# Performance work log

Hardware: AMD Instinct MI355X
Metric: run time of the kernel (lower is better)

## Reference

```python
import jax, jax.numpy as jnp
import numpy as np


def gcn_conv(x, row, col, ew, W, b, N):
    # GCNConv: add self-loops (weight 1), symmetric normalization, X @ W, scatter-add, + bias
    loop = jnp.arange(N, dtype=row.dtype)
    r = jnp.concatenate([row, loop])
    c = jnp.concatenate([col, loop])
    w = jnp.concatenate([ew, jnp.ones((N,), dtype=x.dtype)])
    deg = jax.ops.segment_sum(w, c, num_segments=N)
    dinv = jnp.where(deg > 0, jax.lax.rsqrt(deg), 0.0).astype(x.dtype)
    norm = dinv[r] * w * dinv[c]                  # [E+N]
    h = x @ W                                     # [N, out]
    msg = h[r] * norm[:, None]                    # gather + scale
    out = jax.ops.segment_sum(msg, c, num_segments=N)  # scatter-add to targets
    return out + b


def setup_inputs() -> dict:
    key = jax.random.key(0)
    ks = jax.random.split(key, 10)
    N, E, C_in, C_hid, C_out = 65536, 1048576, 16, 64, 2
    x = jax.random.normal(ks[0], (N, C_in), dtype=jnp.float32)
    edge_index = jax.random.randint(ks[1], (2, E), 0, N, dtype=jnp.int64)
    edge_weight = jax.random.uniform(ks[2], (E,), dtype=jnp.float32)
    s = lambda k, sh, fan: jax.random.normal(k, sh, dtype=jnp.float32) / np.sqrt(fan)
    return {
        "x": x,
        "edge_index": edge_index,
        "edge_weight": edge_weight,
        "W1": s(ks[3], (C_in, C_hid), C_in),
        "b1": jnp.zeros((C_hid,), dtype=jnp.float32),
        "W2": s(ks[4], (C_hid, C_hid), C_hid),
        "b2": jnp.zeros((C_hid,), dtype=jnp.float32),
        "Wl": s(ks[5], (C_hid, C_out), C_hid),
        "bl": jnp.zeros((C_out,), dtype=jnp.float32),
    }


def reference(x, edge_index, edge_weight, W1, b1, W2, b2, Wl, bl):
    N = x.shape[0]
    row, col = edge_index[0], edge_index[1]  # source -> target
    h = jax.nn.relu(gcn_conv(x, row, col, edge_weight, W1, b1, N))
    h = jax.nn.relu(gcn_conv(h, row, col, edge_weight, W2, b2, N))
    return h @ Wl + bl
```

## Files before the change

### kernel.cpp

```cpp
#include <hip/hip_runtime.h>
#include <hip/hip_fp16.h>

#define CHUNK 4096
#define SEGCAP 6144

__device__ __forceinline__ unsigned pack_h2(float a, float b) {
    __half2 h = __floats2half2_rn(a, b);
    return *reinterpret_cast<unsigned*>(&h);
}

__device__ __forceinline__ void scan_boff(const int* __restrict__ bsum, int nb,
                                          int* boff) {
    int t = threadIdx.x;
    int v = (t < nb) ? bsum[t] : 0;
    boff[t] = v;
    __syncthreads();
    for (int o = 1; o < 256; o <<= 1) {
        int x = (t >= o) ? boff[t - o] : 0;
        __syncthreads();
        boff[t] += x;
        __syncthreads();
    }
    int excl = boff[t] - v;
    __syncthreads();
    boff[t] = excl;
    __syncthreads();
}

__global__ __launch_bounds__(256) void s1_hist(const int* __restrict__ col,
                                               int* __restrict__ F, int E, int nsb) {
    __shared__ int cnt[256];
    int t = threadIdx.x, b = blockIdx.x;
    cnt[t] = 0;
    __syncthreads();
    int s = b * CHUNK, e = min(E, s + CHUNK);
    for (int i = s + t; i < e; i += 256) atomicAdd(&cnt[col[i] >> 8], 1);
    __syncthreads();
    F[t * nsb + b] = cnt[t];
}

__global__ void scanF1(int* __restrict__ F, int* __restrict__ bsum, int n) {
    __shared__ int sd[256];
    int t = threadIdx.x, i = blockIdx.x * 256 + t;
    int v = (i < n) ? F[i] : 0;
    sd[t] = v;
    __syncthreads();
    for (int o = 1; o < 256; o <<= 1) {
        int x = (t >= o) ? sd[t - o] : 0;
        __syncthreads();
        sd[t] += x;
        __syncthreads();
    }
    if (i < n) F[i] = sd[t] - v;
    if (t == 255) bsum[blockIdx.x] = sd[255];
}

__global__ __launch_bounds__(256) void s3_scatter(const int* __restrict__ col,
                                                  const int* __restrict__ row,
                                                  const float* __restrict__ ew,
                                                  const int* __restrict__ F,
                                                  const int* __restrict__ bsum,
                                                  int2* __restrict__ tmp, int E, int nsb) {
    __shared__ int boff[256];
    __shared__ int off[256];
    __shared__ int cnt[256];
    __shared__ int lofs[256];
    __shared__ int cur[256];
    __shared__ int2 ed[CHUNK];
    __shared__ unsigned short perm[CHUNK];
    int t = threadIdx.x, b = blockIdx.x;
    scan_boff(bsum, nsb, boff);
    off[t] = F[t * nsb + b] + boff[t];
    cnt[t] = 0; cur[t] = 0;
    __syncthreads();
    int s = b * CHUNK;
    int m = min(E - s, CHUNK);
    for (int i = t; i < m; i += 256) {
        int c = col[s + i];
        ed[i] = make_int2((row[s + i] & 0xFFFF) | (c << 16), __float_as_int(ew[s + i]));
        atomicAdd(&cnt[c >> 8], 1);
    }
    __syncthreads();
    int v = cnt[t];
    lofs[t] = v;
    __syncthreads();
    for (int o = 1; o < 256; o <<= 1) {
        int x = (t >= o) ? lofs[t - o] : 0;
        __syncthreads();
        lofs[t] += x;
        __syncthreads();
    }
    int excl = lofs[t] - v;
    __syncthreads();
    lofs[t] = excl;
    __syncthreads();
    for (int i = t; i < m; i += 256) {
        int bk = ((unsigned)ed[i].x) >> 24;
        int rk = atomicAdd(&cur[bk], 1);
        perm[lofs[bk] + rk] = (unsigned short)i;
    }
    __syncthreads();
    for (int p = t; p < m; p += 256) {
        int2 v2 = ed[perm[p]];
        int bk = ((unsigned)v2.x) >> 24;
        tmp[off[bk] + (p - lofs[bk])] = v2;
    }
}

__global__ __launch_bounds__(256) void s4_fine(const int2* __restrict__ tmp,
                                               const int* __restrict__ F,
                                               const int* __restrict__ bsum,
                                               unsigned* __restrict__ pack,
                                               float* __restrict__ dinv,
                                               int* __restrict__ start,
                                               const float* __restrict__ x,
                                               const float* __restrict__ W1,
                                               __half* __restrict__ g1,
                                               int n, int E, int nsb, int nbuck) {
    __shared__ int   boff[256];
    __shared__ int   fcnt[256];
    __shared__ float fdeg[256];
    __shared__ int   foff[256];
    __shared__ int   fcur[256];
    __shared__ float Ws[16 * 64];
    __shared__ int2  seg[SEGCAP];
    __shared__ unsigned short perm[SEGCAP];
    int t = threadIdx.x, b = blockIdx.x;
    scan_boff(bsum, nsb, boff);
    reinterpret_cast<float4*>(Ws)[t] = reinterpret_cast<const float4*>(W1)[t];
    fcnt[t] = 0; fdeg[t] = 0.f; fcur[t] = 0;
    __syncthreads();
    int segS = F[b * nsb] + boff[b];
    int segE = (b == nbuck - 1) ? E : (F[(b + 1) * nsb] + boff[b + 1]);
    int m = segE - segS;
    if (m <= SEGCAP) {
        for (int i = t; i < m; i += 256) seg[i] = tmp[segS + i];
        __syncthreads();
        for (int i = t; i < m; i += 256) {
            int2 v = seg[i];
            int f = (v.x >> 16) & 255;
            atomicAdd(&fcnt[f], 1);
            atomicAdd(&fdeg[f], __int_as_float(v.y));
        }
        __syncthreads();
        int val = fcnt[t];
        foff[t] = val;
        __syncthreads();
        for (int o = 1; o < 256; o <<= 1) {
            int xk = (t >= o) ? foff[t - o] : 0;
            __syncthreads();
            foff[t] += xk;
            __syncthreads();
        }
        int excl = foff[t] - val;
        __syncthreads();
        foff[t] = excl;
        __syncthreads();
        for (int i = t; i < m; i += 256) {
            int f = (seg[i].x >> 16) & 255;
            int rk = atomicAdd(&fcur[f], 1);
            perm[foff[f] + rk] = (unsigned short)i;
        }
        __syncthreads();
        for (int p = t; p < m; p += 256) {
            int2 v = seg[perm[p]];
            __half hw = __float2half_rn(__int_as_float(v.y));
            pack[segS + p] = (unsigned)(v.x & 0xFFFF) |
                             ((unsigned)*reinterpret_cast<unsigned short*>(&hw) << 16);
        }
    } else {
        for (int i = segS + t; i < segE; i += 256) {
            int2 v = tmp[i];
            int f = (v.x >> 16) & 255;
            atomicAdd(&fcnt[f], 1);
            atomicAdd(&fdeg[f], __int_as_float(v.y));
        }
        __syncthreads();
        int val = fcnt[t];
        foff[t] = val;
        __syncthreads();
        for (int o = 1; o < 256; o <<= 1) {
            int xk = (t >= o) ? foff[t - o] : 0;
            __syncthreads();
            foff[t] += xk;
            __syncthreads();
        }
        int excl = foff[t] - val;
        __syncthreads();
        foff[t] = excl;
        __syncthreads();
        for (int i = segS + t; i < segE; i += 256) {
            int2 v = tmp[i];
            int f = (v.x >> 16) & 255;
            int rk = atomicAdd(&fcur[f], 1);
            __half hw = __float2half_rn(__int_as_float(v.y));
            pack[segS + foff[f] + rk] = (unsigned)(v.x & 0xFFFF) |
                             ((unsigned)*reinterpret_cast<unsigned short*>(&hw) << 16);
        }
    }
    int c = (b << 8) | t;
    float di = rsqrtf(fdeg[t] + 1.0f);
    if (c < n) {
        dinv[c]  = di;
        start[c] = segS + foff[t];
    }
    if (b == nbuck - 1 && t == 255) start[n] = E;
    if (c >= n) return;
    float xv[16];
    const float4* xr = reinterpret_cast<const float4*>(x + (size_t)c * 16);
#pragma unroll
    for (int i = 0; i < 4; ++i)
        *reinterpret_cast<float4*>(&xv[i * 4]) = xr[i];
    uint2* orow = reinterpret_cast<uint2*>(g1 + ((size_t)c << 6));
    for (int jb = 0; jb < 16; ++jb) {
        float4 acc = make_float4(0.f, 0.f, 0.f, 0.f);
#pragma unroll
        for (int k = 0; k < 16; ++k) {
            float hk = xv[k];
            const float4 wv = *reinterpret_cast<const float4*>(&Ws[k * 64 + jb * 4]);
            acc.x += hk * wv.x; acc.y += hk * wv.y;
            acc.z += hk * wv.z; acc.w += hk * wv.w;
        }
        uint2 st;
        st.x = pack_h2(acc.x * di, acc.y * di);
        st.y = pack_h2(acc.z * di, acc.w * di);
        orow[jb] = st;
    }
}

__global__ __launch_bounds__(256) void gemm_hid(const float* __restrict__ h,
                                                const float* __restrict__ W,
                                                const float* __restrict__ dinv,
                                                __half* __restrict__ out, int n) {
    __shared__ float Ws[64 * 64];
    int t = threadIdx.x;
#pragma unroll
    for (int i = 0; i < 16; ++i) Ws[i * 256 + t] = W[i * 256 + t];
    __syncthreads();
    int node = blockIdx.x * 256 + t;
    if (node >= n) return;
    float hv[64];
    const float4* hr = reinterpret_cast<const float4*>(h + ((size_t)node << 6));
#pragma unroll
    for (int i = 0; i < 16; ++i)
        *reinterpret_cast<float4*>(&hv[i * 4]) = hr[i];
    float di = dinv[node];
    uint2* orow = reinterpret_cast<uint2*>(out + ((size_t)node << 6));
    for (int jb = 0; jb < 16; ++jb) {
        float4 acc = make_float4(0.f, 0.f, 0.f, 0.f);
#pragma unroll
        for (int k = 0; k < 64; ++k) {
            float hk = hv[k];
            const float4 wv = *reinterpret_cast<const float4*>(&Ws[k * 64 + jb * 4]);
            acc.x += hk * wv.x; acc.y += hk * wv.y;
            acc.z += hk * wv.z; acc.w += hk * wv.w;
        }
        uint2 st;
        st.x = pack_h2(acc.x * di, acc.y * di);
        st.y = pack_h2(acc.z * di, acc.w * di);
        orow[jb] = st;
    }
}

__device__ __forceinline__ float4 load_row4(const __half* __restrict__ g,
                                            unsigned pk, int ch4, float* wout) {
    unsigned short hw = (unsigned short)(pk >> 16);
    *wout = __half2float(*reinterpret_cast<__half*>(&hw));
    uint2 u = *reinterpret_cast<const uint2*>(g + ((size_t)(pk & 0xFFFFu) << 6) + ch4);
    float2 a = __half22float2(*reinterpret_cast<__half2*>(&u.x));
    float2 b = __half22float2(*reinterpret_cast<__half2*>(&u.y));
    return make_float4(a.x, a.y, b.x, b.y);
}

__device__ __forceinline__ float4 gather_acc(const int* __restrict__ start,
                                             const unsigned* __restrict__ pack,
                                             const __half* __restrict__ g,
                                             int wid, int sub, int ch4) {
    int s = start[wid], e = start[wid + 1];
    float4 acc = make_float4(0.f, 0.f, 0.f, 0.f);
    int i = s;
    for (; i + 7 < e; i += 8) {
        unsigned pa = pack[i + sub];
        unsigned pb = pack[i + 4 + sub];
        float wa, wb;
        float4 va = load_row4(g, pa, ch4, &wa);
        float4 vb = load_row4(g, pb, ch4, &wb);
        acc.x += va.x * wa; acc.y += va.y * wa; acc.z += va.z * wa; acc.w += va.w * wa;
        acc.x += vb.x * wb; acc.y += vb.y * wb; acc.z += vb.z * wb; acc.w += vb.w * wb;
    }
    if (i + 3 < e) {
        unsigned pa = pack[i + sub];
        float wa;
        float4 va = load_row4(g, pa, ch4, &wa);
        acc.x += va.x * wa; acc.y += va.y * wa; acc.z += va.z * wa; acc.w += va.w * wa;
        i += 4;
    }
    int rem = e - i;
    if (sub < rem) {
        unsigned pa = pack[i + sub];
        float wa;
        float4 va = load_row4(g, pa, ch4, &wa);
        acc.x += va.x * wa; acc.y += va.y * wa; acc.z += va.z * wa; acc.w += va.w * wa;
    }
#pragma unroll
    for (int m = 16; m <= 32; m <<= 1) {
        acc.x += __shfl_xor(acc.x, m, 64);
        acc.y += __shfl_xor(acc.y, m, 64);
        acc.z += __shfl_xor(acc.z, m, 64);
        acc.w += __shfl_xor(acc.w, m, 64);
    }
    return acc;
}

__global__ __launch_bounds__(256) void gather_mid(const int* __restrict__ start,
                                                  const unsigned* __restrict__ pack,
                                                  const __half* __restrict__ g,
                                                  const float* __restrict__ dinv,
                                                  const float* __restrict__ b,
                                                  float* __restrict__ out, int n) {
    int wid = (blockIdx.x * blockDim.x + threadIdx.x) >> 6;
    if (wid >= n) return;
    int lane = threadIdx.x & 63;
    int sub = lane >> 4;
    int ch4 = (lane & 15) << 2;
    float4 acc = gather_acc(start, pack, g, wid, sub, ch4);
    if (sub == 0) {
        float di = dinv[wid];
        uint2 u0 = *reinterpret_cast<const uint2*>(g + ((size_t)wid << 6) + ch4);
        float2 ga = __half22float2(*reinterpret_cast<__half2*>(&u0.x));
        float2 gb = __half22float2(*reinterpret_cast<__half2*>(&u0.y));
        const float4 bb = *reinterpret_cast<const float4*>(b + ch4);
        float4 r;
        r.x = fmaxf(di * (acc.x + ga.x) + bb.x, 0.f);
        r.y = fmaxf(di * (acc.y + ga.y) + bb.y, 0.f);
        r.z = fmaxf(di * (acc.z + gb.x) + bb.z, 0.f);
        r.w = fmaxf(di * (acc.w + gb.y) + bb.w, 0.f);
        *reinterpret_cast<float4*>(out + ((size_t)wid << 6) + ch4) = r;
    }
}

__global__ __launch_bounds__(256) void gather_head(const int* __restrict__ start,
                                                   const unsigned* __restrict__ pack,
                                                   const __half* __restrict__ g,
                                                   const float* __restrict__ dinv,
                                                   const float* __restrict__ b,
                                                   const float* __restrict__ Wl,
                                                   const float* __restrict__ bl,
                                                   float* __restrict__ out, int n) {
    int wid = (blockIdx.x * blockDim.x + threadIdx.x) >> 6;
    if (wid >= n) return;
    int lane = threadIdx.x & 63;
    int sub = lane >> 4;
    int ch4 = (lane & 15) << 2;
    float4 acc = gather_acc(start, pack, g, wid, sub, ch4);
    if (sub == 0) {
        float di = dinv[wid];
        uint2 u0 = *reinterpret_cast<const uint2*>(g + ((size_t)wid << 6) + ch4);
        float2 ga = __half22float2(*reinterpret_cast<__half2*>(&u0.x));
        float2 gb = __half22float2(*reinterpret_cast<__half2*>(&u0.y));
        const float4 bb = *reinterpret_cast<const float4*>(b + ch4);
        float4 h;
        h.x = fmaxf(di * (acc.x + ga.x) + bb.x, 0.f);
        h.y = fmaxf(di * (acc.y + ga.y) + bb.y, 0.f);
        h.z = fmaxf(di * (acc.z + gb.x) + bb.z, 0.f);
        h.w = fmaxf(di * (acc.w + gb.y) + bb.w, 0.f);
        float s0 = h.x * Wl[(ch4 + 0) * 2] + h.y * Wl[(ch4 + 1) * 2] +
                   h.z * Wl[(ch4 + 2) * 2] + h.w * Wl[(ch4 + 3) * 2];
        float s1 = h.x * Wl[(ch4 + 0) * 2 + 1] + h.y * Wl[(ch4 + 1) * 2 + 1] +
                   h.z * Wl[(ch4 + 2) * 2 + 1] + h.w * Wl[(ch4 + 3) * 2 + 1];
#pragma unroll
        for (int m = 1; m <= 8; m <<= 1) {
            s0 += __shfl_xor(s0, m, 64);
            s1 += __shfl_xor(s1, m, 64);
        }
        if (lane == 0) {
            out[(size_t)wid * 2 + 0] = s0 + bl[0];
            out[(size_t)wid * 2 + 1] = s1 + bl[1];
        }
    }
}

extern "C" void kernel_launch(void* const* d_in, const int* in_sizes, int n_in,
                              void* d_out, int out_size, void* d_ws, size_t ws_size,
                              hipStream_t stream) {
    const float* x  = (const float*)d_in[0];
    const int*   ei = (const int*)d_in[1];
    const float* ew = (const float*)d_in[2];
    const float* W1 = (const float*)d_in[3];
    const float* b1 = (const float*)d_in[4];
    const float* W2 = (const float*)d_in[5];
    const float* b2 = (const float*)d_in[6];
    const float* Wl = (const float*)d_in[7];
    const float* bl = (const float*)d_in[8];
    float* out = (float*)d_out;

    const int N = in_sizes[0] / 16;
    const int E = in_sizes[2];
    const int* row = ei;
    const int* col = ei + E;
    const int NB    = (N + 255) / 256;
    const int nbuck = N >> 8;
    const int nsb   = (E + CHUNK - 1) / CHUNK;
    const int FSZ   = 256 * nsb;
    const int FB    = (FSZ + 255) / 256;

    char* p = (char*)d_ws;
    unsigned* pack = (unsigned*)p;  p += (size_t)E * 4;
    __half*   bufA = (__half*)p;    p += (size_t)N * 64 * 2;
    char*     r2   = p;             p += (size_t)N * 64 * 4;
    float*    dinv = (float*)p;     p += (size_t)N * 4;
    int*    startO = (int*)p;       p += (size_t)(N + 1) * 4;

    int2* tmp  = (int2*)r2;
    int*  F    = (int*)(r2 + (size_t)E * 8);
    int*  bsum = F + FSZ;
    float* bufB = (float*)r2;

    s1_hist<<<nsb, 256, 0, stream>>>(col, F, E, nsb);
    scanF1<<<FB, 256, 0, stream>>>(F, bsum, FSZ);
    s3_scatter<<<nsb, 256, 0, stream>>>(col, row, ew, F, bsum, tmp, E, nsb);
    s4_fine<<<nbuck, 256, 0, stream>>>(tmp, F, bsum, pack, dinv, startO,
                                       x, W1, bufA, N, E, nsb, nbuck);

    gather_mid<<<(N + 3) / 4, 256, 0, stream>>>(startO, pack, bufA, dinv, b1, bufB, N);

    gemm_hid<<<NB, 256, 0, stream>>>(bufB, W2, dinv, bufA, N);

    gather_head<<<(N + 3) / 4, 256, 0, stream>>>(startO, pack, bufA, dinv, b2, Wl, bl, out, N);
}
```

Measured before the change: 137.7 us.

## Fuse CSR build into cooperative kernel and fold hidden GEMM into gather

Merges the four graph-sorting kernels (histogram, scan, coarse scatter, fine sort with layer-1 GEMM) into one cooperative kernel with grid-wide syncs. This removes launch gaps and the separate scan kernel. It also fuses the layer-2 64x64 GEMM into the first gather kernel using wavefront shuffles, so the fp32 hidden buffer is never written and re-read. The risks are grid.sync overhead, the occupancy limit a cooperative launch imposes (256 blocks with about 64KB of LDS each), and every gather block now reloading 16KB of W2 into LDS.

```diff
diff --git a/kernel.cpp b/kernel.cpp
--- a/kernel.cpp
+++ b/kernel.cpp
@@ -1,5 +1,8 @@
 #include <hip/hip_runtime.h>
 #include <hip/hip_fp16.h>
+#include <hip/hip_cooperative_groups.h>
+
+namespace cg = cooperative_groups;
 
 #define CHUNK 4096
 #define SEGCAP 6144
@@ -9,200 +12,186 @@
     return *reinterpret_cast<unsigned*>(&h);
 }
 
-__device__ __forceinline__ void scan_boff(const int* __restrict__ bsum, int nb,
-                                          int* boff) {
-    int t = threadIdx.x;
-    int v = (t < nb) ? bsum[t] : 0;
-    boff[t] = v;
+__global__ __launch_bounds__(256) void coop_build(
+        const int* __restrict__ col, const int* __restrict__ row,
+        const float* __restrict__ ew,
+        int* __restrict__ F, int* __restrict__ bsum, int2* __restrict__ tmp,
+        unsigned* __restrict__ pack, float* __restrict__ dinv, int* __restrict__ start,
+        const float* __restrict__ x, const float* __restrict__ W1,
+        __half* __restrict__ g1, int n, int E, int nsb, int nbuck) {
+    cg::grid_group grid = cg::this_grid();
+    __shared__ int   boff[256];
+    __shared__ int   a0[256];
+    __shared__ int   a1[256];
+    __shared__ int   a2[256];
+    __shared__ float a3[256];
+    __shared__ float Ws[1024];
+    __shared__ char  big[61440];
+    int t = threadIdx.x, b = blockIdx.x;
+
+    if (b < nsb) {
+        a0[t] = 0;
+        __syncthreads();
+        int s = b * CHUNK, e = min(E, s + CHUNK);
+        for (int i = s + t; i < e; i += 256) atomicAdd(&a0[col[i] >> 8], 1);
+        __syncthreads();
+        F[t * nsb + b] = a0[t];
+    }
+    grid.sync();
+
+    if (b < nbuck) {
+        int v = (t < nsb) ? F[b * nsb + t] : 0;
+        a0[t] = v;
+        __syncthreads();
+        for (int o = 1; o < 256; o <<= 1) {
+            int x2 = (t >= o) ? a0[t - o] : 0;
+            __syncthreads();
+            a0[t] += x2;
+            __syncthreads();
+        }
+        if (t < nsb) F[b * nsb + t] = a0[t] - v;
+        if (t == 255) bsum[b] = a0[255];
+    }
+    grid.sync();
+
+    {
+        int v = (t < nbuck) ? bsum[t] : 0;
+        boff[t] = v;
+        __syncthreads();
+        for (int o = 1; o < 256; o <<= 1) {
+            int x2 = (t >= o) ? boff[t - o] : 0;
+            __syncthreads();
+            boff[t] += x2;
+            __syncthreads();
+        }
+        int excl = boff[t] - v;
+        __syncthreads();
+        boff[t] = excl;
+        __syncthreads();
+    }
+
+    if (b < nsb) {
+        int* off = (int*)a3;
+        off[t] = F[t * nsb + b] + boff[t];
+        a0[t] = 0; a2[t] = 0;
+        __syncthreads();
+        int s = b * CHUNK;
+        int m = min(E - s, CHUNK);
+        int2* ed = (int2*)big;
+        unsigned short* permC = (unsigned short*)(big + sizeof(int2) * CHUNK);
+        for (int i = t; i < m; i += 256) {
+            int c = col[s + i];
+            ed[i] = make_int2((row[s + i] & 0xFFFF) | (c << 16), __float_as_int(ew[s + i]));
+            atomicAdd(&a0[c >> 8], 1);
+        }
+        __syncthreads();
+        int v = a0[t];
+        a1[t] = v;
+        __syncthreads();
+        for (int o = 1; o < 256; o <<= 1) {
+            int x2 = (t >= o) ? a1[t - o] : 0;
+            __syncthreads();
+            a1[t] += x2;
+            __syncthreads();
+        }
+        int excl = a1[t] - v;
+        __syncthreads();
+        a1[t] = excl;
+        __syncthreads();
+        for (int i = t; i < m; i += 256) {
+            int bk = ((unsigned)ed[i].x) >> 24;
+            int rk = atomicAdd(&a2[bk], 1);
+            permC[a1[bk] + rk] = (unsigned short)i;
+        }
+        __syncthreads();
+        for (int p2 = t; p2 < m; p2 += 256) {
+            int2 v2 = ed[permC[p2]];
+            int bk = ((unsigned)v2.x) >> 24;
+            tmp[off[bk] + (p2 - a1[bk])] = v2;
+        }
+    }
+    grid.sync();
+
+    Ws[t] = W1[t]; Ws[256 + t] = W1[256 + t];
+    Ws[512 + t] = W1[512 + t]; Ws[768 + t] = W1[768 + t];
+    if (b >= nbuck) return;
+    a0[t] = 0; a3[t] = 0.f; a2[t] = 0;
     __syncthreads();
-    for (int o = 1; o < 256; o <<= 1) {
-        int x = (t >= o) ? boff[t - o] : 0;
-        __syncthreads();
-        boff[t] += x;
-        __syncthreads();
-    }
-    int excl = boff[t] - v;
-    __syncthreads();
-    boff[t] = excl;
-    __syncthreads();
-}
-
-__global__ __launch_bounds__(256) void s1_hist(const int* __restrict__ col,
-                                               int* __restrict__ F, int E, int nsb) {
-    __shared__ int cnt[256];
-    int t = threadIdx.x, b = blockIdx.x;
-    cnt[t] = 0;
-    __syncthreads();
-    int s = b * CHUNK, e = min(E, s + CHUNK);
-    for (int i = s + t; i < e; i += 256) atomicAdd(&cnt[col[i] >> 8], 1);
-    __syncthreads();
-    F[t * nsb + b] = cnt[t];
-}
-
-__global__ void scanF1(int* __restrict__ F, int* __restrict__ bsum, int n) {
-    __shared__ int sd[256];
-    int t = threadIdx.x, i = blockIdx.x * 256 + t;
-    int v = (i < n) ? F[i] : 0;
-    sd[t] = v;
-    __syncthreads();
-    for (int o = 1; o < 256; o <<= 1) {
-        int x = (t >= o) ? sd[t - o] : 0;
-        __syncthreads();
-        sd[t] += x;
-        __syncthreads();
-    }
-    if (i < n) F[i] = sd[t] - v;
-    if (t == 255) bsum[blockIdx.x] = sd[255];
-}
-
-__global__ __launch_bounds__(256) void s3_scatter(const int* __restrict__ col,
-                                                  const int* __restrict__ row,
-                                                  const float* __restrict__ ew,
-                                                  const int* __restrict__ F,
-                                                  const int* __restrict__ bsum,
-                                                  int2* __restrict__ tmp, int E, int nsb) {
-    __shared__ int boff[256];
-    __shared__ int off[256];
-    __shared__ int cnt[256];
-    __shared__ int lofs[256];
-    __shared__ int cur[256];
-    __shared__ int2 ed[CHUNK];
-    __shared__ unsigned short perm[CHUNK];
-    int t = threadIdx.x, b = blockIdx.x;
-    scan_boff(bsum, nsb, boff);
-    off[t] = F[t * nsb + b] + boff[t];
-    cnt[t] = 0; cur[t] = 0;
-    __syncthreads();
-    int s = b * CHUNK;
-    int m = min(E - s, CHUNK);
-    for (int i = t; i < m; i += 256) {
-        int c = col[s + i];
-        ed[i] = make_int2((row[s + i] & 0xFFFF) | (c << 16), __float_as_int(ew[s + i]));
-        atomicAdd(&cnt[c >> 8], 1);
-    }
-    __syncthreads();
-    int v = cnt[t];
-    lofs[t] = v;
-    __syncthreads();
-    for (int o = 1; o < 256; o <<= 1) {
-        int x = (t >= o) ? lofs[t - o] : 0;
-        __syncthreads();
-        lofs[t] += x;
-        __syncthreads();
-    }
-    int excl = lofs[t] - v;
-    __syncthreads();
-    lofs[t] = excl;
-    __syncthreads();
-    for (int i = t; i < m; i += 256) {
-        int bk = ((unsigned)ed[i].x) >> 24;
-        int rk = atomicAdd(&cur[bk], 1);
-        perm[lofs[bk] + rk] = (unsigned short)i;
-    }
-    __syncthreads();
-    for (int p = t; p < m; p += 256) {
-        int2 v2 = ed[perm[p]];
-        int bk = ((unsigned)v2.x) >> 24;
-        tmp[off[bk] + (p - lofs[bk])] = v2;
-    }
-}
-
-__global__ __launch_bounds__(256) void s4_fine(const int2* __restrict__ tmp,
-                                               const int* __restrict__ F,
-                                               const int* __restrict__ bsum,
-                                               unsigned* __restrict__ pack,
-                                               float* __restrict__ dinv,
-                                               int* __restrict__ start,
-                                               const float* __restrict__ x,
-                                               const float* __restrict__ W1,
-                                               __half* __restrict__ g1,
-                                               int n, int E, int nsb, int nbuck) {
-    __shared__ int   boff[256];
-    __shared__ int   fcnt[256];
-    __shared__ float fdeg[256];
-    __shared__ int   foff[256];
-    __shared__ int   fcur[256];
-    __shared__ float Ws[16 * 64];
-    __shared__ int2  seg[SEGCAP];
-    __shared__ unsigned short perm[SEGCAP];
-    int t = threadIdx.x, b = blockIdx.x;
-    scan_boff(bsum, nsb, boff);
-    reinterpret_cast<float4*>(Ws)[t] = reinterpret_cast<const float4*>(W1)[t];
-    fcnt[t] = 0; fdeg[t] = 0.f; fcur[t] = 0;
-    __syncthreads();
-    int segS = F[b * nsb] + boff[b];
-    int segE = (b == nbuck - 1) ? E : (F[(b + 1) * nsb] + boff[b + 1]);
+    int segS = boff[b];
+    int segE = (b == nbuck - 1) ? E : boff[b + 1];
     int m = segE - segS;
+    int2* seg = (int2*)big;
+    unsigned short* permD = (unsigned short*)(big + sizeof(int2) * SEGCAP);
     if (m <= SEGCAP) {
         for (int i = t; i < m; i += 256) seg[i] = tmp[segS + i];
         __syncthreads();
         for (int i = t; i < m; i += 256) {
             int2 v = seg[i];
             int f = (v.x >> 16) & 255;
-            atomicAdd(&fcnt[f], 1);
-            atomicAdd(&fdeg[f], __int_as_float(v.y));
-        }
-        __syncthreads();
-        int val = fcnt[t];
-        foff[t] = val;
+            atomicAdd(&a0[f], 1);
+            atomicAdd(&a3[f], __int_as_float(v.y));
+        }
+        __syncthreads();
+        int val = a0[t];
+        a1[t] = val;
         __syncthreads();
         for (int o = 1; o < 256; o <<= 1) {
-            int xk = (t >= o) ? foff[t - o] : 0;
-            __syncthreads();
-            foff[t] += xk;
-            __syncthreads();
-        }
-        int excl = foff[t] - val;
-        __syncthreads();
-        foff[t] = excl;
+            int xk = (t >= o) ? a1[t - o] : 0;
+            __syncthreads();
+            a1[t] += xk;
+            __syncthreads();
+        }
+        int excl = a1[t] - val;
+        __syncthreads();
+        a1[t] = excl;
         __syncthreads();
         for (int i = t; i < m; i += 256) {
             int f = (seg[i].x >> 16) & 255;
-            int rk = atomicAdd(&fcur[f], 1);
-            perm[foff[f] + rk] = (unsigned short)i;
-        }
-        __syncthreads();
-        for (int p = t; p < m; p += 256) {
-            int2 v = seg[perm[p]];
+            int rk = atomicAdd(&a2[f], 1);
+            permD[a1[f] + rk] = (unsigned short)i;
+        }
+        __syncthreads();
+        for (int p2 = t; p2 < m; p2 += 256) {
+            int2 v = seg[permD[p2]];
             __half hw = __float2half_rn(__int_as_float(v.y));
-            pack[segS + p] = (unsigned)(v.x & 0xFFFF) |
-                             ((unsigned)*reinterpret_cast<unsigned short*>(&hw) << 16);
+            pack[segS + p2] = (unsigned)(v.x & 0xFFFF) |
+                              ((unsigned)*reinterpret_cast<unsigned short*>(&hw) << 16);
         }
     } else {
         for (int i = segS + t; i < segE; i += 256) {
             int2 v = tmp[i];
             int f = (v.x >> 16) & 255;
-            atomicAdd(&fcnt[f], 1);
-            atomicAdd(&fdeg[f], __int_as_float(v.y));
-        }
-        __syncthreads();
-        int val = fcnt[t];
-        foff[t] = val;
+            atomicAdd(&a0[f], 1);
+            atomicAdd(&a3[f], __int_as_float(v.y));
+        }
+        __syncthreads();
+        int val = a0[t];
+        a1[t] = val;
         __syncthreads();
         for (int o = 1; o < 256; o <<= 1) {
-            int xk = (t >= o) ? foff[t - o] : 0;
-            __syncthreads();
-            foff[t] += xk;
-            __syncthreads();
-        }
-        int excl = foff[t] - val;
-        __syncthreads();
-        foff[t] = excl;
+            int xk = (t >= o) ? a1[t - o] : 0;
+            __syncthreads();
+            a1[t] += xk;
+            __syncthreads();
+        }
+        int excl = a1[t] - val;
+        __syncthreads();
+        a1[t] = excl;
         __syncthreads();
         for (int i = segS + t; i < segE; i += 256) {
             int2 v = tmp[i];
             int f = (v.x >> 16) & 255;
-            int rk = atomicAdd(&fcur[f], 1);
+            int rk = atomicAdd(&a2[f], 1);
             __half hw = __float2half_rn(__int_as_float(v.y));
-            pack[segS + foff[f] + rk] = (unsigned)(v.x & 0xFFFF) |
-                             ((unsigned)*reinterpret_cast<unsigned short*>(&hw) << 16);
+            pack[segS + a1[f] + rk] = (unsigned)(v.x & 0xFFFF) |
+                              ((unsigned)*reinterpret_cast<unsigned short*>(&hw) << 16);
         }
     }
     int c = (b << 8) | t;
-    float di = rsqrtf(fdeg[t] + 1.0f);
+    float di = rsqrtf(a3[t] + 1.0f);
     if (c < n) {
         dinv[c]  = di;
-        start[c] = segS + foff[t];
+        start[c] = segS + a1[t];
     }
     if (b == nbuck - 1 && t == 255) start[n] = E;
     if (c >= n) return;
@@ -217,40 +206,6 @@
 #pragma unroll
         for (int k = 0; k < 16; ++k) {
             float hk = xv[k];
-            const float4 wv = *reinterpret_cast<const float4*>(&Ws[k * 64 + jb * 4]);
-            acc.x += hk * wv.x; acc.y += hk * wv.y;
-            acc.z += hk * wv.z; acc.w += hk * wv.w;
-        }
-        uint2 st;
-        st.x = pack_h2(acc.x * di, acc.y * di);
-        st.y = pack_h2(acc.z * di, acc.w * di);
-        orow[jb] = st;
-    }
-}
-
-__global__ __launch_bounds__(256) void gemm_hid(const float* __restrict__ h,
-                                                const float* __restrict__ W,
-                                                const float* __restrict__ dinv,
-                                                __half* __restrict__ out, int n) {
-    __shared__ float Ws[64 * 64];
-    int t = threadIdx.x;
-#pragma unroll
-    for (int i = 0; i < 16; ++i) Ws[i * 256 + t] = W[i * 256 + t];
-    __syncthreads();
-    int node = blockIdx.x * 256 + t;
-    if (node >= n) return;
-    float hv[64];
-    const float4* hr = reinterpret_cast<const float4*>(h + ((size_t)node << 6));
-#pragma unroll
-    for (int i = 0; i < 16; ++i)
-        *reinterpret_cast<float4*>(&hv[i * 4]) = hr[i];
-    float di = dinv[node];
-    uint2* orow = reinterpret_cast<uint2*>(out + ((size_t)node << 6));
-    for (int jb = 0; jb < 16; ++jb) {
-        float4 acc = make_float4(0.f, 0.f, 0.f, 0.f);
-#pragma unroll
-        for (int k = 0; k < 64; ++k) {
-            float hk = hv[k];
             const float4 wv = *reinterpret_cast<const float4*>(&Ws[k * 64 + jb * 4]);
             acc.x += hk * wv.x; acc.y += hk * wv.y;
             acc.z += hk * wv.z; acc.w += hk * wv.w;
@@ -312,31 +267,51 @@
     return acc;
 }
 
-__global__ __launch_bounds__(256) void gather_mid(const int* __restrict__ start,
-                                                  const unsigned* __restrict__ pack,
-                                                  const __half* __restrict__ g,
-                                                  const float* __restrict__ dinv,
-                                                  const float* __restrict__ b,
-                                                  float* __restrict__ out, int n) {
-    int wid = (blockIdx.x * blockDim.x + threadIdx.x) >> 6;
+__global__ __launch_bounds__(256) void gather_mid_gemm(const int* __restrict__ start,
+                                                       const unsigned* __restrict__ pack,
+                                                       const __half* __restrict__ g,
+                                                       const float* __restrict__ dinv,
+                                                       const float* __restrict__ b1,
+                                                       const float* __restrict__ W2,
+                                                       __half* __restrict__ g2, int n) {
+    __shared__ float Ws[64 * 64];
+    int t = threadIdx.x;
+#pragma unroll
+    for (int i = 0; i < 16; ++i) Ws[i * 256 + t] = W2[i * 256 + t];
+    __syncthreads();
+    int wid = (blockIdx.x * blockDim.x + t) >> 6;
     if (wid >= n) return;
-    int lane = threadIdx.x & 63;
+    int lane = t & 63;
     int sub = lane >> 4;
     int ch4 = (lane & 15) << 2;
     float4 acc = gather_acc(start, pack, g, wid, sub, ch4);
-    if (sub == 0) {
-        float di = dinv[wid];
+    float di = dinv[wid];
+    float4 h4;
+    {
         uint2 u0 = *reinterpret_cast<const uint2*>(g + ((size_t)wid << 6) + ch4);
         float2 ga = __half22float2(*reinterpret_cast<__half2*>(&u0.x));
         float2 gb = __half22float2(*reinterpret_cast<__half2*>(&u0.y));
-        const float4 bb = *reinterpret_cast<const float4*>(b + ch4);
-        float4 r;
-        r.x = fmaxf(di * (acc.x + ga.x) + bb.x, 0.f);
-        r.y = fmaxf(di * (acc.y + ga.y) + bb.y, 0.f);
-        r.z = fmaxf(di * (acc.z + gb.x) + bb.z, 0.f);
-        r.w = fmaxf(di * (acc.w + gb.y) + bb.w, 0.f);
-        *reinterpret_cast<float4*>(out + ((size_t)wid << 6) + ch4) = r;
-    }
+        const float4 bb = *reinterpret_cast<const float4*>(b1 + ch4);
+        h4.x = fmaxf(di * (acc.x + ga.x) + bb.x, 0.f);
+        h4.y = fmaxf(di * (acc.y + ga.y) + bb.y, 0.f);
+        h4.z = fmaxf(di * (acc.z + gb.x) + bb.z, 0.f);
+        h4.w = fmaxf(di * (acc.w + gb.y) + bb.w, 0.f);
+    }
+    float outj = 0.f;
+#pragma unroll
+    for (int q = 0; q < 16; ++q) {
+        float hx = __shfl(h4.x, q, 64);
+        float hy = __shfl(h4.y, q, 64);
+        float hz = __shfl(h4.z, q, 64);
+        float hw = __shfl(h4.w, q, 64);
+        int k = q << 2;
+        outj += hx * Ws[k * 64 + lane] + hy * Ws[(k + 1) * 64 + lane] +
+                hz * Ws[(k + 2) * 64 + lane] + hw * Ws[(k + 3) * 64 + lane];
+    }
+    outj *= di;
+    float nxt = __shfl_down(outj, 1, 64);
+    if (!(lane & 1))
+        reinterpret_cast<unsigned*>(g2 + ((size_t)wid << 6))[lane >> 1] = pack_h2(outj, nxt);
 }
 
 __global__ __launch_bounds__(256) void gather_head(const int* __restrict__ start,
@@ -398,33 +373,33 @@
     const int E = in_sizes[2];
     const int* row = ei;
     const int* col = ei + E;
-    const int NB    = (N + 255) / 256;
     const int nbuck = N >> 8;
     const int nsb   = (E + CHUNK - 1) / CHUNK;
     const int FSZ   = 256 * nsb;
-    const int FB    = (FSZ + 255) / 256;
 
     char* p = (char*)d_ws;
     unsigned* pack = (unsigned*)p;  p += (size_t)E * 4;
-    __half*   bufA = (__half*)p;    p += (size_t)N * 64 * 2;
+    __half*   g1   = (__half*)p;    p += (size_t)N * 64 * 2;
     char*     r2   = p;             p += (size_t)N * 64 * 4;
     float*    dinv = (float*)p;     p += (size_t)N * 4;
     int*    startO = (int*)p;       p += (size_t)(N + 1) * 4;
 
-    int2* tmp  = (int2*)r2;
-    int*  F    = (int*)(r2 + (size_t)E * 8);
-    int*  bsum = F + FSZ;
-    float* bufB = (float*)r2;
-
-    s1_hist<<<nsb, 256, 0, stream>>>(col, F, E, nsb);
-    scanF1<<<FB, 256, 0, stream>>>(F, bsum, FSZ);
-    s3_scatter<<<nsb, 256, 0, stream>>>(col, row, ew, F, bsum, tmp, E, nsb);
-    s4_fine<<<nbuck, 256, 0, stream>>>(tmp, F, bsum, pack, dinv, startO,
-                                       x, W1, bufA, N, E, nsb, nbuck);
-
-    gather_mid<<<(N + 3) / 4, 256, 0, stream>>>(startO, pack, bufA, dinv, b1, bufB, N);
-
-    gemm_hid<<<NB, 256, 0, stream>>>(bufB, W2, dinv, bufA, N);
-
-    gather_head<<<(N + 3) / 4, 256, 0, stream>>>(startO, pack, bufA, dinv, b2, Wl, bl, out, N);
-}
+    int2*   tmp  = (int2*)r2;
+    int*    F    = (int*)(r2 + (size_t)E * 8);
+    int*    bsum = F + FSZ;
+    __half* g2   = (__half*)r2;
+
+    int grid = (nsb > nbuck) ? nsb : nbuck;
+
+    void* args[] = {(void*)&col, (void*)&row, (void*)&ew,
+                    (void*)&F, (void*)&bsum, (void*)&tmp,
+                    (void*)&pack, (void*)&dinv, (void*)&startO,
+                    (void*)&x, (void*)&W1, (void*)&g1,
+                    (void*)&N, (void*)&E, (void*)&nsb, (void*)&nbuck};
+    hipLaunchCooperativeKernel((const void*)coop_build, dim3(grid), dim3(256),
+                               args, 0, stream);
+
+    gather_mid_gemm<<<(N + 3) / 4, 256, 0, stream>>>(startO, pack, g1, dinv, b1, W2, g2, N);
+
+    gather_head<<<(N + 3) / 4, 256, 0, stream>>>(startO, pack, g2, dinv, b2, Wl, bl, out, N);
+}
```

New measurement: 271.4 us. +97.2%, slower.

## Fuse hidden-layer GEMM into first gather kernel via wave shuffles

Applied to the files above, without the earlier changes.

Merges the layer-1 gather/bias/ReLU kernel with the 64x64 hidden GEMM. Each wave broadcasts its gathered 64-float row by shuffles and computes one output channel per lane against W2 held in shared memory, then writes fp16 directly. This drops a kernel launch and the fp32 intermediate round trip to global memory. In exchange every block now loads a 16KB W2 tile into LDS (N/4 blocks) and adds shuffle and LDS traffic per node.

```diff
diff --git a/kernel.cpp b/kernel.cpp
--- a/kernel.cpp
+++ b/kernel.cpp
@@ -228,40 +228,6 @@
     }
 }
 
-__global__ __launch_bounds__(256) void gemm_hid(const float* __restrict__ h,
-                                                const float* __restrict__ W,
-                                                const float* __restrict__ dinv,
-                                                __half* __restrict__ out, int n) {
-    __shared__ float Ws[64 * 64];
-    int t = threadIdx.x;
-#pragma unroll
-    for (int i = 0; i < 16; ++i) Ws[i * 256 + t] = W[i * 256 + t];
-    __syncthreads();
-    int node = blockIdx.x * 256 + t;
-    if (node >= n) return;
-    float hv[64];
-    const float4* hr = reinterpret_cast<const float4*>(h + ((size_t)node << 6));
-#pragma unroll
-    for (int i = 0; i < 16; ++i)
-        *reinterpret_cast<float4*>(&hv[i * 4]) = hr[i];
-    float di = dinv[node];
-    uint2* orow = reinterpret_cast<uint2*>(out + ((size_t)node << 6));
-    for (int jb = 0; jb < 16; ++jb) {
-        float4 acc = make_float4(0.f, 0.f, 0.f, 0.f);
-#pragma unroll
-        for (int k = 0; k < 64; ++k) {
-            float hk = hv[k];
-            const float4 wv = *reinterpret_cast<const float4*>(&Ws[k * 64 + jb * 4]);
-            acc.x += hk * wv.x; acc.y += hk * wv.y;
-            acc.z += hk * wv.z; acc.w += hk * wv.w;
-        }
-        uint2 st;
-        st.x = pack_h2(acc.x * di, acc.y * di);
-        st.y = pack_h2(acc.z * di, acc.w * di);
-        orow[jb] = st;
-    }
-}
-
 __device__ __forceinline__ float4 load_row4(const __half* __restrict__ g,
                                             unsigned pk, int ch4, float* wout) {
     unsigned short hw = (unsigned short)(pk >> 16);
@@ -312,31 +278,51 @@
     return acc;
 }
 
-__global__ __launch_bounds__(256) void gather_mid(const int* __restrict__ start,
-                                                  const unsigned* __restrict__ pack,
-                                                  const __half* __restrict__ g,
-                                                  const float* __restrict__ dinv,
-                                                  const float* __restrict__ b,
-                                                  float* __restrict__ out, int n) {
-    int wid = (blockIdx.x * blockDim.x + threadIdx.x) >> 6;
+__global__ __launch_bounds__(256) void gather_mid_gemm(const int* __restrict__ start,
+                                                       const unsigned* __restrict__ pack,
+                                                       const __half* __restrict__ g,
+                                                       const float* __restrict__ dinv,
+                                                       const float* __restrict__ b1,
+                                                       const float* __restrict__ W2,
+                                                       __half* __restrict__ g2, int n) {
+    __shared__ float Ws[64 * 64];
+    int t = threadIdx.x;
+#pragma unroll
+    for (int i = 0; i < 16; ++i) Ws[i * 256 + t] = W2[i * 256 + t];
+    __syncthreads();
+    int wid = (blockIdx.x * blockDim.x + t) >> 6;
     if (wid >= n) return;
-    int lane = threadIdx.x & 63;
+    int lane = t & 63;
     int sub = lane >> 4;
     int ch4 = (lane & 15) << 2;
     float4 acc = gather_acc(start, pack, g, wid, sub, ch4);
-    if (sub == 0) {
-        float di = dinv[wid];
+    float di = dinv[wid];
+    float4 h4;
+    {
         uint2 u0 = *reinterpret_cast<const uint2*>(g + ((size_t)wid << 6) + ch4);
         float2 ga = __half22float2(*reinterpret_cast<__half2*>(&u0.x));
         float2 gb = __half22float2(*reinterpret_cast<__half2*>(&u0.y));
-        const float4 bb = *reinterpret_cast<const float4*>(b + ch4);
-        float4 r;
-        r.x = fmaxf(di * (acc.x + ga.x) + bb.x, 0.f);
-        r.y = fmaxf(di * (acc.y + ga.y) + bb.y, 0.f);
-        r.z = fmaxf(di * (acc.z + gb.x) + bb.z, 0.f);
-        r.w = fmaxf(di * (acc.w + gb.y) + bb.w, 0.f);
-        *reinterpret_cast<float4*>(out + ((size_t)wid << 6) + ch4) = r;
-    }
+        const float4 bb = *reinterpret_cast<const float4*>(b1 + ch4);
+        h4.x = fmaxf(di * (acc.x + ga.x) + bb.x, 0.f);
+        h4.y = fmaxf(di * (acc.y + ga.y) + bb.y, 0.f);
+        h4.z = fmaxf(di * (acc.z + gb.x) + bb.z, 0.f);
+        h4.w = fmaxf(di * (acc.w + gb.y) + bb.w, 0.f);
+    }
+    float outj = 0.f;
+#pragma unroll
+    for (int q = 0; q < 16; ++q) {
+        float hx = __shfl(h4.x, q, 64);
+        float hy = __shfl(h4.y, q, 64);
+        float hz = __shfl(h4.z, q, 64);
+        float hw = __shfl(h4.w, q, 64);
+        int k = q << 2;
+        outj += hx * Ws[k * 64 + lane] + hy * Ws[(k + 1) * 64 + lane] +
+                hz * Ws[(k + 2) * 64 + lane] + hw * Ws[(k + 3) * 64 + lane];
+    }
+    outj *= di;
+    float nxt = __shfl_down(outj, 1, 64);
+    if (!(lane & 1))
+        reinterpret_cast<unsigned*>(g2 + ((size_t)wid << 6))[lane >> 1] = pack_h2(outj, nxt);
 }
 
 __global__ __launch_bounds__(256) void gather_head(const int* __restrict__ start,
@@ -398,7 +384,6 @@
     const int E = in_sizes[2];
     const int* row = ei;
     const int* col = ei + E;
-    const int NB    = (N + 255) / 256;
     const int nbuck = N >> 8;
     const int nsb   = (E + CHUNK - 1) / CHUNK;
     const int FSZ   = 256 * nsb;
@@ -406,25 +391,23 @@
 
     char* p = (char*)d_ws;
     unsigned* pack = (unsigned*)p;  p += (size_t)E * 4;
-    __half*   bufA = (__half*)p;    p += (size_t)N * 64 * 2;
+    __half*   g1   = (__half*)p;    p += (size_t)N * 64 * 2;
     char*     r2   = p;             p += (size_t)N * 64 * 4;
     float*    dinv = (float*)p;     p += (size_t)N * 4;
     int*    startO = (int*)p;       p += (size_t)(N + 1) * 4;
 
-    int2* tmp  = (int2*)r2;
-    int*  F    = (int*)(r2 + (size_t)E * 8);
-    int*  bsum = F + FSZ;
-    float* bufB = (float*)r2;
+    int2*   tmp  = (int2*)r2;
+    int*    F    = (int*)(r2 + (size_t)E * 8);
+    int*    bsum = F + FSZ;
+    __half* g2   = (__half*)r2;
 
     s1_hist<<<nsb, 256, 0, stream>>>(col, F, E, nsb);
     scanF1<<<FB, 256, 0, stream>>>(F, bsum, FSZ);
     s3_scatter<<<nsb, 256, 0, stream>>>(col, row, ew, F, bsum, tmp, E, nsb);
     s4_fine<<<nbuck, 256, 0, stream>>>(tmp, F, bsum, pack, dinv, startO,
-                                       x, W1, bufA, N, E, nsb, nbuck);
-
-    gather_mid<<<(N + 3) / 4, 256, 0, stream>>>(startO, pack, bufA, dinv, b1, bufB, N);
-
-    gemm_hid<<<NB, 256, 0, stream>>>(bufB, W2, dinv, bufA, N);
-
-    gather_head<<<(N + 3) / 4, 256, 0, stream>>>(startO, pack, bufA, dinv, b2, Wl, bl, out, N);
-}
+                                       x, W1, g1, N, E, nsb, nbuck);
+
+    gather_mid_gemm<<<(N + 3) / 4, 256, 0, stream>>>(startO, pack, g1, dinv, b1, W2, g2, N);
+
+    gather_head<<<(N + 3) / 4, 256, 0, stream>>>(startO, pack, g2, dinv, b2, Wl, bl, out, N);
+}
```

Result: slower. 168.0 us (+22.0%).
